# Kernel tuning notes

Hardware: AMD Instinct MI355X
Metric: run time of the kernel (lower is better)

Reference implementation:

```python
import jax, jax.numpy as jnp
import numpy as np


def _tent(t):
    # linear interpolation kernel max(1-|t|, 0)
    return jnp.maximum(1.0 - jnp.abs(t), 0.0)


def _slice_coeffs(grid, guide):
    """Trilinear slice of bilateral grid at guide-dependent depth.
    grid: [B, C, D, GH, GW], guide: [B, H, W] in [0,1] -> coeffs [B, C, H, W]."""
    B, C, D, GH, GW = grid.shape
    _, H, W = guide.shape
    # continuous grid coords (HDRNet convention)
    gx = (jnp.arange(W, dtype=guide.dtype) + 0.5) * (GW / W)      # [W]
    gy = (jnp.arange(H, dtype=guide.dtype) + 0.5) * (GH / H)      # [H]
    gz = guide * D                                                # [B,H,W]
    fx = jnp.floor(gx - 0.5)
    fy = jnp.floor(gy - 0.5)
    fz = jnp.floor(gz - 0.5)

    def gather(g, z, y, x):
        # g: [C,D,GH,GW]; z,y,x: [B? broadcasted per-batch] -> [C,H,W]
        return g[:, z, y, x]

    coeffs = jnp.zeros((B, C, H, W), dtype=grid.dtype)
    ones_bhw = jnp.ones_like(gz)
    for dz in (0, 1):
        zz = fz + dz                                   # [B,H,W]
        wz = _tent(gz - 0.5 - zz)                      # [B,H,W]
        zc = jnp.clip(zz, 0, D - 1).astype(jnp.int32)
        for dy in (0, 1):
            yy = fy + dy                               # [H]
            wy = _tent(gy - 0.5 - yy)                  # [H]
            yc = jnp.clip(yy, 0, GH - 1).astype(jnp.int32)
            for dx in (0, 1):
                xx = fx + dx                           # [W]
                wx = _tent(gx - 0.5 - xx)              # [W]
                xc = jnp.clip(xx, 0, GW - 1).astype(jnp.int32)
                # broadcast indices to [B,H,W]
                Y = jnp.broadcast_to(yc[None, :, None], zc.shape)
                X = jnp.broadcast_to(xc[None, None, :], zc.shape)
                corner = jax.vmap(gather)(grid, zc, Y, X)   # [B,C,H,W]
                w = wz * wy[None, :, None] * wx[None, None, :]  # [B,H,W]
                coeffs = coeffs + corner * w[:, None, :, :]
    return coeffs


def reference(grid, guide, image):
    B, C, D, GH, GW = grid.shape
    n_out = image.shape[1]               # 3
    n_aff = C // n_out                   # n_in + 1 = 4
    coeffs = _slice_coeffs(grid, guide)  # [B, C, H, W]
    coeffs = coeffs.reshape(B, n_out, n_aff, *image.shape[2:])  # [B,3,4,H,W]
    # per-pixel affine: out_c = sum_i A[c,i] * img_i + A[c, n_in]
    out = jnp.einsum('bcihw,bihw->bchw', coeffs[:, :, : n_aff - 1], image)
    out = out + coeffs[:, :, n_aff - 1]
    return out


def setup_inputs() -> dict:
    key = jax.random.key(0)
    k1, k2, k3 = jax.random.split(key, 3)
    grid = jax.random.normal(k1, (4, 12, 8, 16, 16), dtype=jnp.float32)
    guide = jax.random.uniform(k2, (4, 1024, 1024), dtype=jnp.float32)
    image = jax.random.uniform(k3, (4, 3, 1024, 1024), dtype=jnp.float32)
    return {"grid": grid, "guide": guide, "image": image}
```

## Files before the change

kernel.cpp:

```cpp
#include <hip/hip_runtime.h>


typedef _Float16 h2 __attribute__((ext_vector_type(2)));

static __device__ __forceinline__ float fdot2f(h2 a, h2 b, float c) {
#if __has_builtin(__builtin_amdgcn_fdot2)
    return __builtin_amdgcn_fdot2(a, b, c, false);
#else
    return (float)a.x * (float)b.x + (float)a.y * (float)b.y + c;
#endif
}

static __device__ __forceinline__ h2 bch2(unsigned u) {
    return __builtin_bit_cast(h2, u);
}

static constexpr int C_ = 12, D_ = 8, GH_ = 16, GW_ = 16;
static constexpr int H_ = 1024, W_ = 1024;
static constexpr int HW_ = H_ * W_;
static constexpr int XS = D_ * C_ + 4;

__global__ __launch_bounds__(256) void bsa_v4_kernel(
    const float* __restrict__ grid,
    const float* __restrict__ guide,
    const float* __restrict__ image,
    float* __restrict__ out)
{
    __shared__ unsigned s[GW_ * XS];

    const int bid = blockIdx.x;
    const int y = bid & (H_ - 1);
    const int b = bid >> 10;
    const int t = threadIdx.x;

    const float gyc = (y + 0.5f) * (1.0f / 64.0f) - 0.5f;
    const float fy = floorf(gyc);
    const float ty = gyc - fy;
    const int iy = (int)fy;
    const int y0 = min(max(iy, 0), GH_ - 1);
    const int y1 = min(max(iy + 1, 0), GH_ - 1);

    const int sx = t & 15, sc = t >> 4;
    float sv0[8], sv1[8];
    const float* gb = grid + b * (C_ * D_ * GH_ * GW_);
    if (t < 192) {
        const int base = sc * (D_ * GH_ * GW_) + sx;
#pragma unroll
        for (int z = 0; z < 8; ++z) {
            sv0[z] = gb[base + z * (GH_ * GW_) + y0 * GW_];
            sv1[z] = gb[base + z * (GH_ * GW_) + y1 * GW_];
        }
    }

    const int xp = t << 2;
    const float* gdp = guide + (size_t)bid * W_;
    const float* imp = image + (size_t)b * 3 * HW_ + (size_t)y * W_;
    const float4 gd = *(const float4*)(gdp + xp);
    const float4 ir = *(const float4*)(imp + xp);
    const float4 ig = *(const float4*)(imp + HW_ + xp);
    const float4 ibv = *(const float4*)(imp + 2 * (size_t)HW_ + xp);

    if (t < 192) {
        float a[8];
#pragma unroll
        for (int z = 0; z < 8; ++z)
            a[z] = sv0[z] + ty * (sv1[z] - sv0[z]);
        const int sl = sx * XS + sc;
#pragma unroll
        for (int z = 0; z < 8; ++z) {
            const int zn = (z < 7) ? z + 1 : 7;
            h2 v = {(_Float16)a[z], (_Float16)a[zn]};
            s[sl + z * C_] = __builtin_bit_cast(unsigned, v);
        }
    }
    __syncthreads();

    const float gxc0 = (xp + 0.5f) * (1.0f / 64.0f) - 0.5f;
    const float fx = floorf(gxc0);
    const int ix = (int)fx;
    const int x0 = min(max(ix, 0), GW_ - 1);
    const int x1 = min(max(ix + 1, 0), GW_ - 1);
    const float tx0 = gxc0 - fx;
    const unsigned* sb0 = s + x0 * XS;
    const unsigned* sb1 = s + x1 * XS;

    const float gzv[4] = {gd.x, gd.y, gd.z, gd.w};
    const float rv[4]  = {ir.x, ir.y, ir.z, ir.w};
    const float gv[4]  = {ig.x, ig.y, ig.z, ig.w};
    const float bv[4]  = {ibv.x, ibv.y, ibv.z, ibv.w};
    float o0[4], o1[4], o2[4];

#pragma unroll
    for (int j = 0; j < 4; ++j) {
        const float gz = gzv[j] * (float)D_ - 0.5f;
        const float fz = floorf(gz);
        const int iz = (int)fz;
        const float tz = (iz < 0) ? 0.0f : (gz - fz);
        const int z0 = max(iz, 0);

        const float tx = tx0 + j * (1.0f / 64.0f);
        const float omtx = 1.0f - tx, omtz = 1.0f - tz;
        const h2 wA = {(_Float16)(omtz * omtx), (_Float16)(tz * omtx)};
        const h2 wB = {(_Float16)(omtz * tx),   (_Float16)(tz * tx)};

        const uint4* q0 = (const uint4*)(sb0 + z0 * C_);
        const uint4* q1 = (const uint4*)(sb1 + z0 * C_);
        const uint4 A0 = q0[0], A1 = q0[1], A2 = q0[2];
        const uint4 B0 = q1[0], B1 = q1[1], B2 = q1[2];

        float a0  = fdot2f(bch2(B0.x), wB, fdot2f(bch2(A0.x), wA, 0.0f));
        float a1  = fdot2f(bch2(B0.y), wB, fdot2f(bch2(A0.y), wA, 0.0f));
        float a2  = fdot2f(bch2(B0.z), wB, fdot2f(bch2(A0.z), wA, 0.0f));
        float a3  = fdot2f(bch2(B0.w), wB, fdot2f(bch2(A0.w), wA, 0.0f));
        float a4  = fdot2f(bch2(B1.x), wB, fdot2f(bch2(A1.x), wA, 0.0f));
        float a5  = fdot2f(bch2(B1.y), wB, fdot2f(bch2(A1.y), wA, 0.0f));
        float a6  = fdot2f(bch2(B1.z), wB, fdot2f(bch2(A1.z), wA, 0.0f));
        float a7  = fdot2f(bch2(B1.w), wB, fdot2f(bch2(A1.w), wA, 0.0f));
        float a8  = fdot2f(bch2(B2.x), wB, fdot2f(bch2(A2.x), wA, 0.0f));
        float a9  = fdot2f(bch2(B2.y), wB, fdot2f(bch2(A2.y), wA, 0.0f));
        float a10 = fdot2f(bch2(B2.z), wB, fdot2f(bch2(A2.z), wA, 0.0f));
        float a11 = fdot2f(bch2(B2.w), wB, fdot2f(bch2(A2.w), wA, 0.0f));

        o0[j] = fmaf(a0, rv[j], fmaf(a1, gv[j], fmaf(a2,  bv[j], a3)));
        o1[j] = fmaf(a4, rv[j], fmaf(a5, gv[j], fmaf(a6,  bv[j], a7)));
        o2[j] = fmaf(a8, rv[j], fmaf(a9, gv[j], fmaf(a10, bv[j], a11)));
    }

    float* const ob = out + (size_t)b * 3 * HW_ + (size_t)y * W_ + xp;
    *(float4*)(ob)                   = make_float4(o0[0], o0[1], o0[2], o0[3]);
    *(float4*)(ob + HW_)             = make_float4(o1[0], o1[1], o1[2], o1[3]);
    *(float4*)(ob + 2 * (size_t)HW_) = make_float4(o2[0], o2[1], o2[2], o2[3]);
}

extern "C" void kernel_launch(void* const* d_in, const int* in_sizes, int n_in,
                              void* d_out, int out_size, void* d_ws, size_t ws_size,
                              hipStream_t stream) {
    const float* grid  = (const float*)d_in[0];
    const float* guide = (const float*)d_in[1];
    const float* image = (const float*)d_in[2];
    float* out = (float*)d_out;
    (void)d_ws; (void)ws_size;

    bsa_v4_kernel<<<4 * H_, 256, 0, stream>>>(grid, guide, image, out);
}
```

Measured before the change: 24.52 us.

## Process four rows per block with register prefetch of next row

Each block now handles four consecutive image rows instead of one. It reuses the grid values loaded once per block and rebuilds the shared y-interpolated slice between rows, separated by barriers. Guide and image loads for the next row are issued before the current row's compute to overlap memory latency. The cost is four times fewer blocks, which means less parallelism to hide memory latency, plus extra barriers per row.

```diff
diff --git a/kernel.cpp b/kernel.cpp
--- a/kernel.cpp
+++ b/kernel.cpp
@@ -19,8 +19,9 @@
 static constexpr int H_ = 1024, W_ = 1024;
 static constexpr int HW_ = H_ * W_;
 static constexpr int XS = D_ * C_ + 4;
+static constexpr int R_ = 4;
 
-__global__ __launch_bounds__(256) void bsa_v4_kernel(
+__global__ __launch_bounds__(256) void bsa_pipe4_kernel(
     const float* __restrict__ grid,
     const float* __restrict__ guide,
     const float* __restrict__ image,
@@ -28,17 +29,18 @@
 {
     __shared__ unsigned s[GW_ * XS];
 
-    const int bid = blockIdx.x;
-    const int y = bid & (H_ - 1);
-    const int b = bid >> 10;
+    const int row0 = blockIdx.x * R_;
+    const int y00 = row0 & (H_ - 1);
+    const int b = row0 >> 10;
     const int t = threadIdx.x;
+    const int xp = t << 2;
 
-    const float gyc = (y + 0.5f) * (1.0f / 64.0f) - 0.5f;
+    const float gyc = (y00 + 0.5f) * (1.0f / 64.0f) - 0.5f;
     const float fy = floorf(gyc);
-    const float ty = gyc - fy;
+    const float ty0 = gyc - fy;
     const int iy = (int)fy;
-    const int y0 = min(max(iy, 0), GH_ - 1);
-    const int y1 = min(max(iy + 1, 0), GH_ - 1);
+    const int yA = min(max(iy, 0), GH_ - 1);
+    const int yB = min(max(iy + 1, 0), GH_ - 1);
 
     const int sx = t & 15, sc = t >> 4;
     float sv0[8], sv1[8];
@@ -47,24 +49,26 @@
         const int base = sc * (D_ * GH_ * GW_) + sx;
 #pragma unroll
         for (int z = 0; z < 8; ++z) {
-            sv0[z] = gb[base + z * (GH_ * GW_) + y0 * GW_];
-            sv1[z] = gb[base + z * (GH_ * GW_) + y1 * GW_];
+            sv0[z] = gb[base + z * (GH_ * GW_) + yA * GW_];
+            sv1[z] = gb[base + z * (GH_ * GW_) + yB * GW_];
         }
     }
 
-    const int xp = t << 2;
-    const float* gdp = guide + (size_t)bid * W_;
-    const float* imp = image + (size_t)b * 3 * HW_ + (size_t)y * W_;
-    const float4 gd = *(const float4*)(gdp + xp);
-    const float4 ir = *(const float4*)(imp + xp);
-    const float4 ig = *(const float4*)(imp + HW_ + xp);
-    const float4 ibv = *(const float4*)(imp + 2 * (size_t)HW_ + xp);
+    const float* gdp = guide + (size_t)b * HW_;
+    const float* imp = image + (size_t)b * 3 * HW_;
+    float* const op  = out   + (size_t)b * 3 * HW_;
+
+    const size_t r0 = (size_t)y00 * W_ + xp;
+    float4 cur_gd = *(const float4*)(gdp + r0);
+    float4 cur_ir = *(const float4*)(imp + r0);
+    float4 cur_ig = *(const float4*)(imp + HW_ + r0);
+    float4 cur_ib = *(const float4*)(imp + 2 * (size_t)HW_ + r0);
 
     if (t < 192) {
         float a[8];
 #pragma unroll
         for (int z = 0; z < 8; ++z)
-            a[z] = sv0[z] + ty * (sv1[z] - sv0[z]);
+            a[z] = sv0[z] + ty0 * (sv1[z] - sv0[z]);
         const int sl = sx * XS + sc;
 #pragma unroll
         for (int z = 0; z < 8; ++z) {
@@ -84,52 +88,87 @@
     const unsigned* sb0 = s + x0 * XS;
     const unsigned* sb1 = s + x1 * XS;
 
-    const float gzv[4] = {gd.x, gd.y, gd.z, gd.w};
-    const float rv[4]  = {ir.x, ir.y, ir.z, ir.w};
-    const float gv[4]  = {ig.x, ig.y, ig.z, ig.w};
-    const float bv[4]  = {ibv.x, ibv.y, ibv.z, ibv.w};
-    float o0[4], o1[4], o2[4];
+#pragma unroll
+    for (int r = 0; r < R_; ++r) {
+        const int y = y00 + r;
+
+        float4 nxt_gd, nxt_ir, nxt_ig, nxt_ib;
+        if (r + 1 < R_) {
+            const size_t rn = (size_t)(y + 1) * W_ + xp;
+            nxt_gd = *(const float4*)(gdp + rn);
+            nxt_ir = *(const float4*)(imp + rn);
+            nxt_ig = *(const float4*)(imp + HW_ + rn);
+            nxt_ib = *(const float4*)(imp + 2 * (size_t)HW_ + rn);
+        }
+
+        const float gzv[4] = {cur_gd.x, cur_gd.y, cur_gd.z, cur_gd.w};
+        const float rv[4]  = {cur_ir.x, cur_ir.y, cur_ir.z, cur_ir.w};
+        const float gv[4]  = {cur_ig.x, cur_ig.y, cur_ig.z, cur_ig.w};
+        const float bv[4]  = {cur_ib.x, cur_ib.y, cur_ib.z, cur_ib.w};
+        float o0[4], o1[4], o2[4];
 
 #pragma unroll
-    for (int j = 0; j < 4; ++j) {
-        const float gz = gzv[j] * (float)D_ - 0.5f;
-        const float fz = floorf(gz);
-        const int iz = (int)fz;
-        const float tz = (iz < 0) ? 0.0f : (gz - fz);
-        const int z0 = max(iz, 0);
+        for (int j = 0; j < 4; ++j) {
+            const float gz = gzv[j] * (float)D_ - 0.5f;
+            const float fz = floorf(gz);
+            const int iz = (int)fz;
+            const float tz = (iz < 0) ? 0.0f : (gz - fz);
+            const int z0 = max(iz, 0);
 
-        const float tx = tx0 + j * (1.0f / 64.0f);
-        const float omtx = 1.0f - tx, omtz = 1.0f - tz;
-        const h2 wA = {(_Float16)(omtz * omtx), (_Float16)(tz * omtx)};
-        const h2 wB = {(_Float16)(omtz * tx),   (_Float16)(tz * tx)};
+            const float tx = tx0 + j * (1.0f / 64.0f);
+            const float omtx = 1.0f - tx, omtz = 1.0f - tz;
+            const h2 wA = {(_Float16)(omtz * omtx), (_Float16)(tz * omtx)};
+            const h2 wB = {(_Float16)(omtz * tx),   (_Float16)(tz * tx)};
 
-        const uint4* q0 = (const uint4*)(sb0 + z0 * C_);
-        const uint4* q1 = (const uint4*)(sb1 + z0 * C_);
-        const uint4 A0 = q0[0], A1 = q0[1], A2 = q0[2];
-        const uint4 B0 = q1[0], B1 = q1[1], B2 = q1[2];
+            const uint4* q0 = (const uint4*)(sb0 + z0 * C_);
+            const uint4* q1 = (const uint4*)(sb1 + z0 * C_);
+            const uint4 A0 = q0[0], A1 = q0[1], A2 = q0[2];
+            const uint4 B0 = q1[0], B1 = q1[1], B2 = q1[2];
 
-        float a0  = fdot2f(bch2(B0.x), wB, fdot2f(bch2(A0.x), wA, 0.0f));
-        float a1  = fdot2f(bch2(B0.y), wB, fdot2f(bch2(A0.y), wA, 0.0f));
-        float a2  = fdot2f(bch2(B0.z), wB, fdot2f(bch2(A0.z), wA, 0.0f));
-        float a3  = fdot2f(bch2(B0.w), wB, fdot2f(bch2(A0.w), wA, 0.0f));
-        float a4  = fdot2f(bch2(B1.x), wB, fdot2f(bch2(A1.x), wA, 0.0f));
-        float a5  = fdot2f(bch2(B1.y), wB, fdot2f(bch2(A1.y), wA, 0.0f));
-        float a6  = fdot2f(bch2(B1.z), wB, fdot2f(bch2(A1.z), wA, 0.0f));
-        float a7  = fdot2f(bch2(B1.w), wB, fdot2f(bch2(A1.w), wA, 0.0f));
-        float a8  = fdot2f(bch2(B2.x), wB, fdot2f(bch2(A2.x), wA, 0.0f));
-        float a9  = fdot2f(bch2(B2.y), wB, fdot2f(bch2(A2.y), wA, 0.0f));
-        float a10 = fdot2f(bch2(B2.z), wB, fdot2f(bch2(A2.z), wA, 0.0f));
-        float a11 = fdot2f(bch2(B2.w), wB, fdot2f(bch2(A2.w), wA, 0.0f));
+            float a0  = fdot2f(bch2(B0.x), wB, fdot2f(bch2(A0.x), wA, 0.0f));
+            float a1  = fdot2f(bch2(B0.y), wB, fdot2f(bch2(A0.y), wA, 0.0f));
+            float a2  = fdot2f(bch2(B0.z), wB, fdot2f(bch2(A0.z), wA, 0.0f));
+            float a3  = fdot2f(bch2(B0.w), wB, fdot2f(bch2(A0.w), wA, 0.0f));
+            float a4  = fdot2f(bch2(B1.x), wB, fdot2f(bch2(A1.x), wA, 0.0f));
+            float a5  = fdot2f(bch2(B1.y), wB, fdot2f(bch2(A1.y), wA, 0.0f));
+            float a6  = fdot2f(bch2(B1.z), wB, fdot2f(bch2(A1.z), wA, 0.0f));
+            float a7  = fdot2f(bch2(B1.w), wB, fdot2f(bch2(A1.w), wA, 0.0f));
+            float a8  = fdot2f(bch2(B2.x), wB, fdot2f(bch2(A2.x), wA, 0.0f));
+            float a9  = fdot2f(bch2(B2.y), wB, fdot2f(bch2(A2.y), wA, 0.0f));
+            float a10 = fdot2f(bch2(B2.z), wB, fdot2f(bch2(A2.z), wA, 0.0f));
+            float a11 = fdot2f(bch2(B2.w), wB, fdot2f(bch2(A2.w), wA, 0.0f));
 
-        o0[j] = fmaf(a0, rv[j], fmaf(a1, gv[j], fmaf(a2,  bv[j], a3)));
-        o1[j] = fmaf(a4, rv[j], fmaf(a5, gv[j], fmaf(a6,  bv[j], a7)));
-        o2[j] = fmaf(a8, rv[j], fmaf(a9, gv[j], fmaf(a10, bv[j], a11)));
+            o0[j] = fmaf(a0, rv[j], fmaf(a1, gv[j], fmaf(a2,  bv[j], a3)));
+            o1[j] = fmaf(a4, rv[j], fmaf(a5, gv[j], fmaf(a6,  bv[j], a7)));
+            o2[j] = fmaf(a8, rv[j], fmaf(a9, gv[j], fmaf(a10, bv[j], a11)));
+        }
+
+        float* const ob = op + (size_t)y * W_ + xp;
+        *(float4*)(ob)                   = make_float4(o0[0], o0[1], o0[2], o0[3]);
+        *(float4*)(ob + HW_)             = make_float4(o1[0], o1[1], o1[2], o1[3]);
+        *(float4*)(ob + 2 * (size_t)HW_) = make_float4(o2[0], o2[1], o2[2], o2[3]);
+
+        __syncthreads();
+        if (r + 1 < R_) {
+            if (t < 192) {
+                const float tyr = ty0 + (r + 1) * (1.0f / 64.0f);
+                float a[8];
+#pragma unroll
+                for (int z = 0; z < 8; ++z)
+                    a[z] = sv0[z] + tyr * (sv1[z] - sv0[z]);
+                const int sl = sx * XS + sc;
+#pragma unroll
+                for (int z = 0; z < 8; ++z) {
+                    const int zn = (z < 7) ? z + 1 : 7;
+                    h2 v = {(_Float16)a[z], (_Float16)a[zn]};
+                    s[sl + z * C_] = __builtin_bit_cast(unsigned, v);
+                }
+            }
+            __syncthreads();
+            cur_gd = nxt_gd; cur_ir = nxt_ir;
+            cur_ig = nxt_ig; cur_ib = nxt_ib;
+        }
     }
-
-    float* const ob = out + (size_t)b * 3 * HW_ + (size_t)y * W_ + xp;
-    *(float4*)(ob)                   = make_float4(o0[0], o0[1], o0[2], o0[3]);
-    *(float4*)(ob + HW_)             = make_float4(o1[0], o1[1], o1[2], o1[3]);
-    *(float4*)(ob + 2 * (size_t)HW_) = make_float4(o2[0], o2[1], o2[2], o2[3]);
 }
 
 extern "C" void kernel_launch(void* const* d_in, const int* in_sizes, int n_in,
@@ -141,5 +180,5 @@
     float* out = (float*)d_out;
     (void)d_ws; (void)ws_size;
 
-    bsa_v4_kernel<<<4 * H_, 256, 0, stream>>>(grid, guide, image, out);
+    bsa_pipe4_kernel<<<(4 * H_) / R_, 256, 0, stream>>>(grid, guide, image, out);
 }
```

After: 24.15 us. About the same (-1.5%).
